# Optimization experiments

Hardware: AMD Instinct MI355X
Metric: run time of the kernel (lower is better)

## Reference

```python
import jax, jax.numpy as jnp
import numpy as np

EPS = 1e-5
NUM_HEADS = 16


def activation_quant(x):
    # 8-bit activation quant with straight-through estimator
    scale = 127.0 / jnp.clip(jnp.max(jnp.abs(x), axis=-1, keepdims=True), 1e-5, None)
    y = jnp.clip(jnp.round(x * scale), -128.0, 127.0) / scale
    return x + jax.lax.stop_gradient(y - x)


def weight_quant(w):
    # ternary {-1,0,1} weight quant with STE
    scale = 1.0 / jnp.clip(jnp.mean(jnp.abs(w)), 1e-5, None)
    wq = jnp.clip(jnp.round(w * scale), -1.0, 1.0) / scale
    return w + jax.lax.stop_gradient(wq - w)


def bitlinear(x, w):
    # F.layer_norm(x, x.shape[1:]): normalize over ALL dims except batch, no affine
    axes = tuple(range(1, x.ndim))
    mu = jnp.mean(x, axis=axes, keepdims=True)
    var = jnp.var(x, axis=axes, keepdims=True)
    xn = (x - mu) * jax.lax.rsqrt(var + EPS)
    return jnp.einsum('bnd,od->bno', activation_quant(xn), weight_quant(w))


def layer_norm(x, gamma, beta):
    mu = jnp.mean(x, axis=-1, keepdims=True)
    var = jnp.var(x, axis=-1, keepdims=True)
    return (x - mu) * jax.lax.rsqrt(var + EPS) * gamma + beta


def setup_inputs() -> dict:
    key = jax.random.key(0)
    k0, k1, k2 = jax.random.split(key, 3)
    B, N, D = 2, 2048, 1024
    return {
        't': jnp.zeros((1,), jnp.float32),
        'x': jax.random.normal(k0, (B, N, D), jnp.float32),
        'w_qkv': jax.random.normal(k1, (3 * D, D), jnp.float32) * 0.02,
        'w_out': jax.random.normal(k2, (D, D), jnp.float32) * 0.02,
        'gamma': jnp.ones((D,), jnp.float32),
        'beta': jnp.zeros((D,), jnp.float32),
    }


def reference(t, x, w_qkv, w_out, gamma, beta):
    B, N, D = x.shape
    H = NUM_HEADS
    hd = D // H
    scale = hd ** -0.5
    h = layer_norm(x, gamma, beta)                     # [B,N,D]
    qkv = bitlinear(h, w_qkv).reshape(B, N, 3, H, hd)   # [B,N,3,H,hd]
    qkv = jnp.transpose(qkv, (2, 0, 3, 1, 4))           # [3,B,H,N,hd]
    q, k, v = qkv[0], qkv[1], qkv[2]
    attn = jax.nn.softmax(jnp.einsum('bhnd,bhmd->bhnm', q, k) * scale, axis=-1)
    out = jnp.einsum('bhnm,bhmd->bhnd', attn, v)        # [B,H,N,hd]
    out = jnp.transpose(out, (0, 2, 1, 3)).reshape(B, N, D)
    return bitlinear(out, w_out)
```

## Files before the change

### kernel.cpp

```cpp
#include <hip/hip_runtime.h>
#include <hip/hip_bf16.h>
#include <hip/hip_fp16.h>
#include <math.h>

typedef __hip_bfloat16 bf16;
typedef int   i32x4 __attribute__((ext_vector_type(4)));
typedef float f32x4 __attribute__((ext_vector_type(4)));
typedef short bfx8  __attribute__((ext_vector_type(8)));

#define EPSV 1e-5f
#define NROWS 4096
#define DIM   1024
#define NSEQ  2048

__device__ __forceinline__ float ldv(const void* p, size_t i, int dt){
  if (dt == 0) return ((const float*)p)[i];
  if (dt == 1) return __bfloat162float(((const bf16*)p)[i]);
  return __half2float(((const __half*)p)[i]);
}

__device__ __forceinline__ float blk_sum(float v, float* sm){
  #pragma unroll
  for (int o = 32; o > 0; o >>= 1) v += __shfl_xor(v, o, 64);
  __syncthreads();
  if ((threadIdx.x & 63) == 0) sm[threadIdx.x >> 6] = v;
  __syncthreads();
  return sm[0] + sm[1] + sm[2] + sm[3];
}
__device__ __forceinline__ double blk_sum_d(double v, double* sm){
  #pragma unroll
  for (int o = 32; o > 0; o >>= 1) v += __shfl_xor(v, o, 64);
  __syncthreads();
  if ((threadIdx.x & 63) == 0) sm[threadIdx.x >> 6] = v;
  __syncthreads();
  return sm[0] + sm[1] + sm[2] + sm[3];
}
__device__ __forceinline__ float blk_max(float v, float* sm){
  #pragma unroll
  for (int o = 32; o > 0; o >>= 1) v = fmaxf(v, __shfl_xor(v, o, 64));
  __syncthreads();
  if ((threadIdx.x & 63) == 0) sm[threadIdx.x >> 6] = v;
  __syncthreads();
  return fmaxf(fmaxf(sm[0], sm[1]), fmaxf(sm[2], sm[3]));
}

__global__ void setup_gb(const void* c0, const void* c1, int* flags,
                         float* gamma_f, float* beta_f){
  __shared__ int sdt, sgf;
  if (threadIdx.x == 0){
    unsigned u0 = *(const unsigned*)c0;
    int gfirst = (u0 != 0u) ? 1 : 0;
    const unsigned short* g = (const unsigned short*)(gfirst ? c0 : c1);
    int dt;
    if (g[0] == 0x3F80) dt = 1;
    else if (g[0] == 0x3C00) dt = 2;
    else dt = 0;
    flags[0] = dt; flags[1] = gfirst;
    sdt = dt; sgf = gfirst;
  }
  __syncthreads();
  int dt = sdt;
  const void* g = sgf ? c0 : c1;
  const void* b = sgf ? c1 : c0;
  for (int i = threadIdx.x; i < DIM; i += blockDim.x){
    gamma_f[i] = ldv(g, i, dt);
    beta_f[i]  = ldv(b, i, dt);
  }
}

__global__ __launch_bounds__(256) void ln_rows(const void* __restrict__ x,
                                               const float* __restrict__ gamma_f,
                                               const float* __restrict__ beta_f,
                                               float* __restrict__ h,
                                               double* __restrict__ lnp,
                                               const int* __restrict__ flags){
  __shared__ float sm[4];
  __shared__ double smd[4];
  int dt = flags[0];
  int row = blockIdx.x;
  int tid = threadIdx.x;
  float v[4]; float s = 0.f;
  if (dt == 0){
    float4 v4 = ((const float4*)x)[(size_t)row*256 + tid];
    v[0]=v4.x; v[1]=v4.y; v[2]=v4.z; v[3]=v4.w;
  } else {
    size_t base = (size_t)row * DIM;
    #pragma unroll
    for (int i = 0; i < 4; ++i) v[i] = ldv(x, base + 4*tid + i, dt);
  }
  #pragma unroll
  for (int i = 0; i < 4; ++i) s += v[i];
  s = blk_sum(s, sm);
  float mu = s * (1.f/1024.f);
  float d2 = 0.f;
  #pragma unroll
  for (int i = 0; i < 4; ++i){ float d = v[i] - mu; d2 += d*d; }
  d2 = blk_sum(d2, sm);
  float rs = rsqrtf(d2 * (1.f/1024.f) + EPSV);
  float4 gm = ((const float4*)gamma_f)[tid];
  float4 bt = ((const float4*)beta_f)[tid];
  float hv[4];
  hv[0] = (v[0]-mu)*rs*gm.x + bt.x;
  hv[1] = (v[1]-mu)*rs*gm.y + bt.y;
  hv[2] = (v[2]-mu)*rs*gm.z + bt.z;
  hv[3] = (v[3]-mu)*rs*gm.w + bt.w;
  ((float4*)h)[(size_t)row*256 + tid] = make_float4(hv[0],hv[1],hv[2],hv[3]);
  double hs = 0.0, hq = 0.0;
  #pragma unroll
  for (int i = 0; i < 4; ++i){ hs += (double)hv[i]; hq += (double)hv[i]*(double)hv[i]; }
  hs = blk_sum_d(hs, smd);
  hq = blk_sum_d(hq, smd);
  if (tid == 0){ lnp[2*row] = hs; lnp[2*row + 1] = hq; }
}

__global__ __launch_bounds__(256) void abs_reduce(const void* __restrict__ w, int n,
                                                  double* __restrict__ part,
                                                  const int* __restrict__ flags){
  __shared__ double smd[4];
  int dt = flags[0];
  double s = 0.0;
  if (dt == 0){
    const float4* w4 = (const float4*)w;
    int n4 = n >> 2;
    for (int i = blockIdx.x*256 + threadIdx.x; i < n4; i += gridDim.x*256){
      float4 v = w4[i];
      s += (double)(fabsf(v.x) + fabsf(v.y)) + (double)(fabsf(v.z) + fabsf(v.w));
    }
  } else {
    for (int i = blockIdx.x*256 + threadIdx.x; i < n; i += gridDim.x*256)
      s += (double)fabsf(ldv(w, i, dt));
  }
  s = blk_sum_d(s, smd);
  if (threadIdx.x == 0) part[blockIdx.x] = s;
}

__global__ __launch_bounds__(256) void finalize1(float* acc,
                                                 const double* __restrict__ lnp,
                                                 const double* __restrict__ awp1,
                                                 const double* __restrict__ awp2){
  __shared__ double smd[4];
  int tid = threadIdx.x;
  double s0=0, q0=0, s1=0, q1=0, a1=0, a2=0;
  for (int i = tid; i < 2048; i += 256){
    s0 += lnp[2*i];          q0 += lnp[2*i + 1];
    s1 += lnp[2*(i+2048)];   q1 += lnp[2*(i+2048) + 1];
  }
  for (int i = tid; i < 512; i += 256){ a1 += awp1[i]; a2 += awp2[i]; }
  s0 = blk_sum_d(s0, smd);  q0 = blk_sum_d(q0, smd);
  s1 = blk_sum_d(s1, smd);  q1 = blk_sum_d(q1, smd);
  a1 = blk_sum_d(a1, smd);  a2 = blk_sum_d(a2, smd);
  if (tid == 0){
    const double cnt = 2097152.0;
    double mu0 = s0/cnt, var0 = q0/cnt - mu0*mu0;
    double mu1 = s1/cnt, var1 = q1/cnt - mu1*mu1;
    acc[16] = (float)mu0; acc[17] = (float)(1.0 / sqrt(var0 + 1e-5));
    acc[18] = (float)mu1; acc[19] = (float)(1.0 / sqrt(var1 + 1e-5));
    acc[20] = (float)(1.0 / fmax(a1 / (3.0*1024.0*1024.0), 1e-5));
    acc[21] = (float)(1.0 / fmax(a2 / (1024.0*1024.0), 1e-5));
  }
}

__global__ __launch_bounds__(256) void finalize2(float* acc,
                                                 const double* __restrict__ atp){
  __shared__ double smd[4];
  int tid = threadIdx.x;
  double s0 = atp[2*tid],        q0 = atp[2*tid + 1];
  double s1 = atp[2*(256+tid)],  q1 = atp[2*(256+tid) + 1];
  s0 = blk_sum_d(s0, smd);  q0 = blk_sum_d(q0, smd);
  s1 = blk_sum_d(s1, smd);  q1 = blk_sum_d(q1, smd);
  if (tid == 0){
    const double cnt = 2097152.0;
    double mu0 = s0/cnt, var0 = q0/cnt - mu0*mu0;
    double mu1 = s1/cnt, var1 = q1/cnt - mu1*mu1;
    acc[22] = (float)mu0; acc[23] = (float)(1.0 / sqrt(var0 + 1e-5));
    acc[24] = (float)mu1; acc[25] = (float)(1.0 / sqrt(var1 + 1e-5));
  }
}

__global__ __launch_bounds__(256) void act_quant_i8(const float* __restrict__ buf,
                                                    signed char* __restrict__ qout,
                                                    float* __restrict__ rscale,
                                                    const float* __restrict__ acc,
                                                    int statOff){
  __shared__ float sm[4];
  int row = blockIdx.x;
  int b = row >> 11;
  float mu = acc[statOff + 2*b], rs = acc[statOff + 2*b + 1];
  int tid = threadIdx.x;
  float4 v4 = ((const float4*)buf)[(size_t)row*256 + tid];
  float v[4] = {(v4.x-mu)*rs, (v4.y-mu)*rs, (v4.z-mu)*rs, (v4.w-mu)*rs};
  float am = fmaxf(fmaxf(fabsf(v[0]), fabsf(v[1])), fmaxf(fabsf(v[2]), fabsf(v[3])));
  am = blk_max(am, sm);
  am = fmaxf(am, 1e-5f);
  float s127 = 127.f / am;
  unsigned pk = 0;
  #pragma unroll
  for (int i = 0; i < 4; ++i){
    float q = rintf(v[i] * s127);
    q = fminf(fmaxf(q, -128.f), 127.f);
    pk |= ((unsigned)(unsigned char)(signed char)q) << (8*i);
  }
  ((unsigned*)qout)[(size_t)row*256 + tid] = pk;
  if (tid == 0) rscale[row] = am * (1.f/127.f);
}

__global__ __launch_bounds__(256) void w_quant_i8(const void* __restrict__ w,
                                                  signed char* __restrict__ wq, int n,
                                                  const float* __restrict__ acc, int sidx,
                                                  const int* __restrict__ flags){
  int dt = flags[0];
  float scale = acc[sidx];
  if (dt == 0){
    const float4* w4 = (const float4*)w;
    int n4 = n >> 2;
    for (int i = blockIdx.x*256 + threadIdx.x; i < n4; i += gridDim.x*256){
      float4 v = w4[i];
      float vv[4] = {v.x, v.y, v.z, v.w};
      unsigned pk = 0;
      #pragma unroll
      for (int j = 0; j < 4; ++j){
        float q = rintf(vv[j] * scale);
        q = fminf(fmaxf(q, -1.f), 1.f);
        pk |= ((unsigned)(unsigned char)(signed char)q) << (8*j);
      }
      ((unsigned*)wq)[i] = pk;
    }
  } else {
    for (int i = blockIdx.x*256 + threadIdx.x; i < n; i += gridDim.x*256){
      float q = rintf(ldv(w, i, dt) * scale);
      q = fminf(fmaxf(q, -1.f), 1.f);
      wq[i] = (signed char)q;
    }
  }
}

__global__ __launch_bounds__(256) void gemm_i8(const signed char* __restrict__ A,
                                               const signed char* __restrict__ W,
                                               const float* __restrict__ rscale,
                                               const float* __restrict__ acc, int sidx,
                                               float* __restrict__ Cf,
                                               bf16* __restrict__ Cb,
                                               int ldc, int writeBf, float q_prescale){
  __shared__ __attribute__((aligned(16))) signed char Asl[128][80];
  __shared__ __attribute__((aligned(16))) signed char Bsl[128][80];
  int tid = threadIdx.x, lane = tid & 63, w = tid >> 6;
  int wr = w >> 1, wc = w & 1;

  int nwgx = gridDim.x;
  int flat = blockIdx.y * nwgx + blockIdx.x;
  int nwg  = nwgx * gridDim.y;
  int cpx  = nwg >> 3;
  int swz  = (flat & 7) * cpx + (flat >> 3);
  int r0 = (swz / nwgx) * 128, o0 = (swz % nwgx) * 128;

  i32x4 zz = {0,0,0,0};
  i32x4 accv[4][4];
  #pragma unroll
  for (int m = 0; m < 4; ++m)
    #pragma unroll
    for (int n = 0; n < 4; ++n) accv[m][n] = zz;

  int sr0 = tid >> 2, sr1 = sr0 + 64;
  int sc  = (tid & 3) * 16;

  i32x4 a0, a1, b0, b1;
  a0 = *(const i32x4*)(A + (size_t)(r0 + sr0)*1024 + sc);
  a1 = *(const i32x4*)(A + (size_t)(r0 + sr1)*1024 + sc);
  b0 = *(const i32x4*)(W + (size_t)(o0 + sr0)*1024 + sc);
  b1 = *(const i32x4*)(W + (size_t)(o0 + sr1)*1024 + sc);

  for (int k0 = 0; k0 < 1024; k0 += 64){
    __syncthreads();
    *(i32x4*)&Asl[sr0][sc] = a0;
    *(i32x4*)&Asl[sr1][sc] = a1;
    *(i32x4*)&Bsl[sr0][sc] = b0;
    *(i32x4*)&Bsl[sr1][sc] = b1;
    __syncthreads();
    if (k0 + 64 < 1024){
      int kn = k0 + 64;
      a0 = *(const i32x4*)(A + (size_t)(r0 + sr0)*1024 + kn + sc);
      a1 = *(const i32x4*)(A + (size_t)(r0 + sr1)*1024 + kn + sc);
      b0 = *(const i32x4*)(W + (size_t)(o0 + sr0)*1024 + kn + sc);
      b1 = *(const i32x4*)(W + (size_t)(o0 + sr1)*1024 + kn + sc);
    }
    i32x4 af[4], bfr[4];
    #pragma unroll
    for (int m = 0; m < 4; ++m)
      af[m] = *(const i32x4*)&Asl[wr*64 + m*16 + (lane & 15)][(lane >> 4) * 16];
    #pragma unroll
    for (int n = 0; n < 4; ++n)
      bfr[n] = *(const i32x4*)&Bsl[wc*64 + n*16 + (lane & 15)][(lane >> 4) * 16];
    #pragma unroll
    for (int m = 0; m < 4; ++m)
      #pragma unroll
      for (int n = 0; n < 4; ++n)
        accv[m][n] = __builtin_amdgcn_mfma_i32_16x16x64_i8(af[m], bfr[n], accv[m][n], 0, 0, 0);
  }

  float wsc = acc[sidx];
  float cs = (o0 < 1024) ? q_prescale : 1.0f;
  float rf[4][4];
  #pragma unroll
  for (int m = 0; m < 4; ++m)
    #pragma unroll
    for (int r = 0; r < 4; ++r)
      rf[m][r] = rscale[r0 + wr*64 + m*16 + ((lane >> 4) << 2) + r] / wsc * cs;

  #pragma unroll
  for (int m = 0; m < 4; ++m)
    #pragma unroll
    for (int n = 0; n < 4; ++n)
      #pragma unroll
      for (int r = 0; r < 4; ++r){
        float val = (float)accv[m][n][r] * rf[m][r];
        size_t row = (size_t)(r0 + wr*64 + m*16 + ((lane >> 4) << 2) + r);
        int col = o0 + wc*64 + n*16 + (lane & 15);
        if (writeBf) Cb[row * ldc + col] = __float2bfloat16(val);
        else         Cf[row * ldc + col] = val;
      }
}

__global__ __launch_bounds__(256) void attn_mfma(const bf16* __restrict__ qkv,
                                                 float* __restrict__ out,
                                                 double* __restrict__ atp){
  __shared__ __attribute__((aligned(16))) unsigned short K_lds[64][72];
  __shared__ __attribute__((aligned(16))) unsigned short Vt_lds[64][72];
  __shared__ __attribute__((aligned(16))) unsigned short P_lds[4][32][72];
  __shared__ double smd[4];

  int tid = threadIdx.x, lane = tid & 63, w = tid >> 6;
  int l15 = lane & 15, g = lane >> 4;
  int bh = blockIdx.y;
  int b = bh >> 4, h = bh & 15;
  int n0 = blockIdx.x * 128;
  const unsigned short* qg = (const unsigned short*)qkv;

  bfx8 qf[2][2];
  #pragma unroll
  for (int qt = 0; qt < 2; ++qt)
    #pragma unroll
    for (int s = 0; s < 2; ++s){
      int qrow = b*NSEQ + n0 + w*32 + qt*16 + l15;
      qf[qt][s] = *(const bfx8*)(qg + (size_t)qrow*3072 + h*64 + g*8 + s*32);
    }

  float m_run[2] = {-INFINITY, -INFINITY};
  float l_run[2] = {0.f, 0.f};
  f32x4 zf = {0.f, 0.f, 0.f, 0.f};
  f32x4 acco[2][4];
  #pragma unroll
  for (int qt = 0; qt < 2; ++qt)
    #pragma unroll
    for (int n = 0; n < 4; ++n) acco[qt][n] = zf;

  int krow = lane;
  int r2 = tid & 31, dwin = tid >> 5;

  bfx8 kc0, kc1, vv0, vv1;
  auto LOADT = [&](int kt){
    size_t kvb = (size_t)(b*NSEQ + kt*64);
    kc0 = *(const bfx8*)(qg + (kvb + krow)*3072 + 1024 + h*64 + w*8);
    kc1 = *(const bfx8*)(qg + (kvb + krow)*3072 + 1024 + h*64 + (w + 4)*8);
    vv0 = *(const bfx8*)(qg + (kvb + 2*r2    )*3072 + 2048 + h*64 + dwin*8);
    vv1 = *(const bfx8*)(qg + (kvb + 2*r2 + 1)*3072 + 2048 + h*64 + dwin*8);
  };
  LOADT(0);

  for (int kt = 0; kt < NSEQ/64; ++kt){
    __syncthreads();
    *(bfx8*)&K_lds[krow][w*8]      = kc0;
    *(bfx8*)&K_lds[krow][w*8 + 32] = kc1;
    #pragma unroll
    for (int u = 0; u < 8; ++u){
      unsigned word = (unsigned)(unsigned short)vv0[u] |
                      ((unsigned)(unsigned short)vv1[u] << 16);
      *(unsigned*)&Vt_lds[dwin*8 + u][2*r2] = word;
    }
    __syncthreads();
    if (kt + 1 < NSEQ/64) LOADT(kt + 1);

    f32x4 sacc[2][4];
    #pragma unroll
    for (int qt = 0; qt < 2; ++qt)
      #pragma unroll
      for (int f = 0; f < 4; ++f) sacc[qt][f] = zf;
    #pragma unroll
    for (int f = 0; f < 4; ++f)
      #pragma unroll
      for (int s = 0; s < 2; ++s){
        bfx8 kb = *(const bfx8*)&K_lds[f*16 + l15][g*8 + s*32];
        sacc[0][f] = __builtin_amdgcn_mfma_f32_16x16x32_bf16(kb, qf[0][s], sacc[0][f], 0, 0, 0);
        sacc[1][f] = __builtin_amdgcn_mfma_f32_16x16x32_bf16(kb, qf[1][s], sacc[1][f], 0, 0, 0);
      }

    #pragma unroll
    for (int qt = 0; qt < 2; ++qt){
      float pm = sacc[qt][0][0];
      #pragma unroll
      for (int f = 0; f < 4; ++f)
        #pragma unroll
        for (int r = 0; r < 4; ++r) pm = fmaxf(pm, sacc[qt][f][r]);
      pm = fmaxf(pm, __shfl_xor(pm, 16, 64));
      pm = fmaxf(pm, __shfl_xor(pm, 32, 64));
      float mnew = fmaxf(m_run[qt], pm);
      float corr = __expf(m_run[qt] - mnew);
      m_run[qt] = mnew;
      float p[4][4]; float ts = 0.f;
      #pragma unroll
      for (int f = 0; f < 4; ++f)
        #pragma unroll
        for (int r = 0; r < 4; ++r){
          p[f][r] = __expf(sacc[qt][f][r] - mnew);
          ts += p[f][r];
        }
      ts += __shfl_xor(ts, 16, 64);
      ts += __shfl_xor(ts, 32, 64);
      l_run[qt] = l_run[qt] * corr + ts;
      #pragma unroll
      for (int f = 0; f < 4; ++f)
        #pragma unroll
        for (int rp = 0; rp < 2; ++rp){
          bf16 pb0 = __float2bfloat16(p[f][2*rp]);
          bf16 pb1 = __float2bfloat16(p[f][2*rp+1]);
          unsigned pk = (unsigned)*reinterpret_cast<unsigned short*>(&pb0) |
                        ((unsigned)*reinterpret_cast<unsigned short*>(&pb1) << 16);
          *(unsigned*)&P_lds[w][qt*16 + l15][16*f + 4*g + 2*rp] = pk;
        }
      float ca[4];
      #pragma unroll
      for (int r = 0; r < 4; ++r) ca[r] = __shfl(corr, 4*g + r, 64);
      #pragma unroll
      for (int n = 0; n < 4; ++n)
        #pragma unroll
        for (int r = 0; r < 4; ++r) acco[qt][n][r] *= ca[r];
    }

    bfx8 pa[2][2];
    #pragma unroll
    for (int qt = 0; qt < 2; ++qt)
      #pragma unroll
      for (int s = 0; s < 2; ++s)
        pa[qt][s] = *(const bfx8*)&P_lds[w][qt*16 + l15][g*8 + s*32];
    #pragma unroll
    for (int n = 0; n < 4; ++n)
      #pragma unroll
      for (int s = 0; s < 2; ++s){
        bfx8 vb = *(const bfx8*)&Vt_lds[n*16 + l15][g*8 + s*32];
        acco[0][n] = __builtin_amdgcn_mfma_f32_16x16x32_bf16(pa[0][s], vb, acco[0][n], 0, 0, 0);
        acco[1][n] = __builtin_amdgcn_mfma_f32_16x16x32_bf16(pa[1][s], vb, acco[1][n], 0, 0, 0);
      }
  }

  float ila[2][4];
  #pragma unroll
  for (int qt = 0; qt < 2; ++qt){
    float il = 1.f / l_run[qt];
    #pragma unroll
    for (int r = 0; r < 4; ++r) ila[qt][r] = __shfl(il, 4*g + r, 64);
  }
  double ssum = 0.0, ssq = 0.0;
  #pragma unroll
  for (int qt = 0; qt < 2; ++qt)
    #pragma unroll
    for (int n = 0; n < 4; ++n)
      #pragma unroll
      for (int r = 0; r < 4; ++r){
        float o = acco[qt][n][r] * ila[qt][r];
        int orow = b*NSEQ + n0 + w*32 + qt*16 + 4*g + r;
        out[(size_t)orow * DIM + h*64 + n*16 + l15] = o;
        ssum += (double)o; ssq += (double)o * (double)o;
      }
  ssum = blk_sum_d(ssum, smd);
  ssq  = blk_sum_d(ssq, smd);
  if (tid == 0){
    int bflat = blockIdx.y * gridDim.x + blockIdx.x;
    atp[2*bflat] = ssum; atp[2*bflat + 1] = ssq;
  }
}

extern "C" void kernel_launch(void* const* d_in, const int* in_sizes, int n_in,
                              void* d_out, int out_size, void* d_ws, size_t ws_size,
                              hipStream_t stream) {
  int ix = -1, iwq = -1, iwo = -1, ig0 = -1, ig1 = -1;
  for (int i = 0; i < n_in; ++i){
    int s = in_sizes[i];
    if      (s == 4194304) ix  = i;
    else if (s == 3145728) iwq = i;
    else if (s == 1048576) iwo = i;
    else if (s == 1024){ if (ig0 < 0) ig0 = i; else ig1 = i; }
  }
  if (ix < 0 || iwq < 0 || iwo < 0 || ig0 < 0 || ig1 < 0){ ix=1; iwq=2; iwo=3; ig0=4; ig1=5; }
  const void* x     = d_in[ix];
  const void* w_qkv = d_in[iwq];
  const void* w_out = d_in[iwo];
  const void* g0    = d_in[ig0];
  const void* g1    = d_in[ig1];

  char* ws = (char*)d_ws;
  float*  acc     = (float*)ws;
  int*    flags   = (int*)(ws + 448);
  float*  gamma_f = (float*)(ws + 4096);
  float*  beta_f  = (float*)(ws + 8192);
  float*  rscale1 = (float*)(ws + 12288);
  float*  rscale2 = (float*)(ws + 28672);
  double* lnp     = (double*)(ws + 65536);
  double* awp1    = (double*)(ws + 131072);
  double* awp2    = (double*)(ws + 135168);
  double* atp     = (double*)(ws + 139264);
  float*        h      = (float*)      (ws + (1u<<20));
  signed char*  h_i8   = (signed char*)(ws + (17u<<20));
  signed char*  wqk_i8 = (signed char*)(ws + (21u<<20));
  signed char*  wqo_i8 = (signed char*)(ws + (24u<<20));
  bf16*         qkvb   = (bf16*)       (ws + (25u<<20));
  signed char*  a2_i8  = (signed char*)(ws + (49u<<20));
  float*        aout   = h;

  setup_gb<<<1, 256, 0, stream>>>(g0, g1, flags, gamma_f, beta_f);
  ln_rows<<<NROWS, 256, 0, stream>>>(x, gamma_f, beta_f, h, lnp, flags);
  abs_reduce<<<512, 256, 0, stream>>>(w_qkv, 3*DIM*DIM, awp1, flags);
  abs_reduce<<<512, 256, 0, stream>>>(w_out, DIM*DIM, awp2, flags);
  finalize1<<<1, 256, 0, stream>>>(acc, lnp, awp1, awp2);
  act_quant_i8<<<NROWS, 256, 0, stream>>>(h, h_i8, rscale1, acc, 16);
  w_quant_i8<<<512, 256, 0, stream>>>(w_qkv, wqk_i8, 3*DIM*DIM, acc, 20, flags);
  w_quant_i8<<<512, 256, 0, stream>>>(w_out, wqo_i8, DIM*DIM, acc, 21, flags);
  gemm_i8<<<dim3(24, 32), 256, 0, stream>>>(h_i8, wqk_i8, rscale1, acc, 20,
                                            nullptr, qkvb, 3072, 1, 0.125f);
  attn_mfma<<<dim3(16, 32), 256, 0, stream>>>(qkvb, aout, atp);
  finalize2<<<1, 256, 0, stream>>>(acc, atp);
  act_quant_i8<<<NROWS, 256, 0, stream>>>(aout, a2_i8, rscale2, acc, 22);
  gemm_i8<<<dim3(8, 32), 256, 0, stream>>>(a2_i8, wqo_i8, rscale2, acc, 21,
                                           (float*)d_out, nullptr, 1024, 0, 1.0f);
}
```

Measured before the change: 171.9 us.

## Halve attention query tile, remap blocks for L2 locality, add lazy rescaling

The attention kernel now handles 64 query rows per block instead of 128, doubling the grid to 1024 blocks and cutting per-wave registers. Block indices are remapped so that consecutive blocks spread across head groups, aiming for better cache reuse of K/V. The online-softmax max and rescale now happen only when some row's max grows by more than 8, which skips most exp/rescale work per tile. Each K/V tile is loaded twice as many times overall, and finalize2 is updated to reduce the larger partial array.

```diff
diff --git a/kernel.cpp b/kernel.cpp
--- a/kernel.cpp
+++ b/kernel.cpp
@@ -164,8 +164,11 @@
                                                  const double* __restrict__ atp){
   __shared__ double smd[4];
   int tid = threadIdx.x;
-  double s0 = atp[2*tid],        q0 = atp[2*tid + 1];
-  double s1 = atp[2*(256+tid)],  q1 = atp[2*(256+tid) + 1];
+  double s0=0, q0=0, s1=0, q1=0;
+  for (int i = tid; i < 512; i += 256){
+    s0 += atp[2*i];          q0 += atp[2*i + 1];
+    s1 += atp[2*(i+512)];    q1 += atp[2*(i+512) + 1];
+  }
   s0 = blk_sum_d(s0, smd);  q0 = blk_sum_d(q0, smd);
   s1 = blk_sum_d(s1, smd);  q1 = blk_sum_d(q1, smd);
   if (tid == 0){
@@ -325,33 +328,32 @@
                                                  double* __restrict__ atp){
   __shared__ __attribute__((aligned(16))) unsigned short K_lds[64][72];
   __shared__ __attribute__((aligned(16))) unsigned short Vt_lds[64][72];
-  __shared__ __attribute__((aligned(16))) unsigned short P_lds[4][32][72];
+  __shared__ __attribute__((aligned(16))) unsigned short P_lds[4][16][72];
   __shared__ double smd[4];
 
   int tid = threadIdx.x, lane = tid & 63, w = tid >> 6;
   int l15 = lane & 15, g = lane >> 4;
-  int bh = blockIdx.y;
+
+  int flat = blockIdx.y * 32 + blockIdx.x;
+  int slot = flat & 7, idx = flat >> 3;
+  int bh = slot * 4 + (idx >> 5);
+  int qx = idx & 31;
   int b = bh >> 4, h = bh & 15;
-  int n0 = blockIdx.x * 128;
+  int n0 = qx * 64;
   const unsigned short* qg = (const unsigned short*)qkv;
 
-  bfx8 qf[2][2];
-  #pragma unroll
-  for (int qt = 0; qt < 2; ++qt)
-    #pragma unroll
-    for (int s = 0; s < 2; ++s){
-      int qrow = b*NSEQ + n0 + w*32 + qt*16 + l15;
-      qf[qt][s] = *(const bfx8*)(qg + (size_t)qrow*3072 + h*64 + g*8 + s*32);
-    }
-
-  float m_run[2] = {-INFINITY, -INFINITY};
-  float l_run[2] = {0.f, 0.f};
+  bfx8 qf[2];
+  #pragma unroll
+  for (int s = 0; s < 2; ++s){
+    int qrow = b*NSEQ + n0 + w*16 + l15;
+    qf[s] = *(const bfx8*)(qg + (size_t)qrow*3072 + h*64 + g*8 + s*32);
+  }
+
+  float m_run = -INFINITY, l_run = 0.f;
   f32x4 zf = {0.f, 0.f, 0.f, 0.f};
-  f32x4 acco[2][4];
-  #pragma unroll
-  for (int qt = 0; qt < 2; ++qt)
-    #pragma unroll
-    for (int n = 0; n < 4; ++n) acco[qt][n] = zf;
+  f32x4 acco[4];
+  #pragma unroll
+  for (int n = 0; n < 4; ++n) acco[n] = zf;
 
   int krow = lane;
   int r2 = tid & 31, dwin = tid >> 5;
@@ -379,101 +381,91 @@
     __syncthreads();
     if (kt + 1 < NSEQ/64) LOADT(kt + 1);
 
-    f32x4 sacc[2][4];
-    #pragma unroll
-    for (int qt = 0; qt < 2; ++qt)
-      #pragma unroll
-      for (int f = 0; f < 4; ++f) sacc[qt][f] = zf;
+    f32x4 sacc[4];
+    #pragma unroll
+    for (int f = 0; f < 4; ++f) sacc[f] = zf;
     #pragma unroll
     for (int f = 0; f < 4; ++f)
       #pragma unroll
       for (int s = 0; s < 2; ++s){
         bfx8 kb = *(const bfx8*)&K_lds[f*16 + l15][g*8 + s*32];
-        sacc[0][f] = __builtin_amdgcn_mfma_f32_16x16x32_bf16(kb, qf[0][s], sacc[0][f], 0, 0, 0);
-        sacc[1][f] = __builtin_amdgcn_mfma_f32_16x16x32_bf16(kb, qf[1][s], sacc[1][f], 0, 0, 0);
+        sacc[f] = __builtin_amdgcn_mfma_f32_16x16x32_bf16(kb, qf[s], sacc[f], 0, 0, 0);
       }
 
-    #pragma unroll
-    for (int qt = 0; qt < 2; ++qt){
-      float pm = sacc[qt][0][0];
-      #pragma unroll
-      for (int f = 0; f < 4; ++f)
-        #pragma unroll
-        for (int r = 0; r < 4; ++r) pm = fmaxf(pm, sacc[qt][f][r]);
-      pm = fmaxf(pm, __shfl_xor(pm, 16, 64));
-      pm = fmaxf(pm, __shfl_xor(pm, 32, 64));
-      float mnew = fmaxf(m_run[qt], pm);
-      float corr = __expf(m_run[qt] - mnew);
-      m_run[qt] = mnew;
-      float p[4][4]; float ts = 0.f;
-      #pragma unroll
-      for (int f = 0; f < 4; ++f)
-        #pragma unroll
-        for (int r = 0; r < 4; ++r){
-          p[f][r] = __expf(sacc[qt][f][r] - mnew);
-          ts += p[f][r];
-        }
-      ts += __shfl_xor(ts, 16, 64);
-      ts += __shfl_xor(ts, 32, 64);
-      l_run[qt] = l_run[qt] * corr + ts;
-      #pragma unroll
-      for (int f = 0; f < 4; ++f)
-        #pragma unroll
-        for (int rp = 0; rp < 2; ++rp){
-          bf16 pb0 = __float2bfloat16(p[f][2*rp]);
-          bf16 pb1 = __float2bfloat16(p[f][2*rp+1]);
-          unsigned pk = (unsigned)*reinterpret_cast<unsigned short*>(&pb0) |
-                        ((unsigned)*reinterpret_cast<unsigned short*>(&pb1) << 16);
-          *(unsigned*)&P_lds[w][qt*16 + l15][16*f + 4*g + 2*rp] = pk;
-        }
+    float pm = sacc[0][0];
+    #pragma unroll
+    for (int f = 0; f < 4; ++f)
+      #pragma unroll
+      for (int r = 0; r < 4; ++r) pm = fmaxf(pm, sacc[f][r]);
+    pm = fmaxf(pm, __shfl_xor(pm, 16, 64));
+    pm = fmaxf(pm, __shfl_xor(pm, 32, 64));
+    if (__any(pm > m_run + 8.f)){
+      float mnew = fmaxf(m_run, pm);
+      float corr = __expf(m_run - mnew);
+      m_run = mnew;
+      l_run *= corr;
       float ca[4];
       #pragma unroll
       for (int r = 0; r < 4; ++r) ca[r] = __shfl(corr, 4*g + r, 64);
       #pragma unroll
       for (int n = 0; n < 4; ++n)
         #pragma unroll
-        for (int r = 0; r < 4; ++r) acco[qt][n][r] *= ca[r];
-    }
-
-    bfx8 pa[2][2];
-    #pragma unroll
-    for (int qt = 0; qt < 2; ++qt)
-      #pragma unroll
-      for (int s = 0; s < 2; ++s)
-        pa[qt][s] = *(const bfx8*)&P_lds[w][qt*16 + l15][g*8 + s*32];
+        for (int r = 0; r < 4; ++r) acco[n][r] *= ca[r];
+    }
+    float p[4][4]; float ts = 0.f;
+    #pragma unroll
+    for (int f = 0; f < 4; ++f)
+      #pragma unroll
+      for (int r = 0; r < 4; ++r){
+        p[f][r] = __expf(sacc[f][r] - m_run);
+        ts += p[f][r];
+      }
+    ts += __shfl_xor(ts, 16, 64);
+    ts += __shfl_xor(ts, 32, 64);
+    l_run += ts;
+
+    #pragma unroll
+    for (int f = 0; f < 4; ++f)
+      #pragma unroll
+      for (int rp = 0; rp < 2; ++rp){
+        bf16 pb0 = __float2bfloat16(p[f][2*rp]);
+        bf16 pb1 = __float2bfloat16(p[f][2*rp+1]);
+        unsigned pk = (unsigned)*reinterpret_cast<unsigned short*>(&pb0) |
+                      ((unsigned)*reinterpret_cast<unsigned short*>(&pb1) << 16);
+        *(unsigned*)&P_lds[w][l15][16*f + 4*g + 2*rp] = pk;
+      }
+
+    bfx8 pa[2];
+    #pragma unroll
+    for (int s = 0; s < 2; ++s)
+      pa[s] = *(const bfx8*)&P_lds[w][l15][g*8 + s*32];
     #pragma unroll
     for (int n = 0; n < 4; ++n)
       #pragma unroll
       for (int s = 0; s < 2; ++s){
         bfx8 vb = *(const bfx8*)&Vt_lds[n*16 + l15][g*8 + s*32];
-        acco[0][n] = __builtin_amdgcn_mfma_f32_16x16x32_bf16(pa[0][s], vb, acco[0][n], 0, 0, 0);
-        acco[1][n] = __builtin_amdgcn_mfma_f32_16x16x32_bf16(pa[1][s], vb, acco[1][n], 0, 0, 0);
+        acco[n] = __builtin_amdgcn_mfma_f32_16x16x32_bf16(pa[s], vb, acco[n], 0, 0, 0);
       }
   }
 
-  float ila[2][4];
-  #pragma unroll
-  for (int qt = 0; qt < 2; ++qt){
-    float il = 1.f / l_run[qt];
-    #pragma unroll
-    for (int r = 0; r < 4; ++r) ila[qt][r] = __shfl(il, 4*g + r, 64);
-  }
+  float il = 1.f / l_run;
+  float ila[4];
+  #pragma unroll
+  for (int r = 0; r < 4; ++r) ila[r] = __shfl(il, 4*g + r, 64);
   double ssum = 0.0, ssq = 0.0;
   #pragma unroll
-  for (int qt = 0; qt < 2; ++qt)
-    #pragma unroll
-    for (int n = 0; n < 4; ++n)
-      #pragma unroll
-      for (int r = 0; r < 4; ++r){
-        float o = acco[qt][n][r] * ila[qt][r];
-        int orow = b*NSEQ + n0 + w*32 + qt*16 + 4*g + r;
-        out[(size_t)orow * DIM + h*64 + n*16 + l15] = o;
-        ssum += (double)o; ssq += (double)o * (double)o;
-      }
+  for (int n = 0; n < 4; ++n)
+    #pragma unroll
+    for (int r = 0; r < 4; ++r){
+      float o = acco[n][r] * ila[r];
+      int orow = b*NSEQ + n0 + w*16 + 4*g + r;
+      out[(size_t)orow * DIM + h*64 + n*16 + l15] = o;
+      ssum += (double)o; ssq += (double)o * (double)o;
+    }
   ssum = blk_sum_d(ssum, smd);
   ssq  = blk_sum_d(ssq, smd);
   if (tid == 0){
-    int bflat = blockIdx.y * gridDim.x + blockIdx.x;
+    int bflat = bh * 32 + qx;
     atp[2*bflat] = ssum; atp[2*bflat + 1] = ssq;
   }
 }
@@ -525,7 +517,7 @@
   w_quant_i8<<<512, 256, 0, stream>>>(w_out, wqo_i8, DIM*DIM, acc, 21, flags);
   gemm_i8<<<dim3(24, 32), 256, 0, stream>>>(h_i8, wqk_i8, rscale1, acc, 20,
                                             nullptr, qkvb, 3072, 1, 0.125f);
-  attn_mfma<<<dim3(16, 32), 256, 0, stream>>>(qkvb, aout, atp);
+  attn_mfma<<<dim3(32, 32), 256, 0, stream>>>(qkvb, aout, atp);
   finalize2<<<1, 256, 0, stream>>>(acc, atp);
   act_quant_i8<<<NROWS, 256, 0, stream>>>(aout, a2_i8, rscale2, acc, 22);
   gemm_i8<<<dim3(8, 32), 256, 0, stream>>>(a2_i8, wqo_i8, rscale2, acc, 21,
```

After: 169.2 us. No clear change (-1.6%).
